# Kernel tuning notes

Hardware: AMD Instinct MI355X
Metric: run time of the kernel (lower is better)

Reference implementation:

```python
import jax, jax.numpy as jnp
import numpy as np

BETA = 0.25
EMA_DECAY = 0.99
EMA_EPS = 1e-05
K = 8192
D = 512


def setup_inputs() -> dict:
    key = jax.random.key(0)
    k1, k2, k3, k4 = jax.random.split(key, 4)
    z = jax.random.normal(k1, (8, 2048, D), dtype=jnp.float32)
    codebook_weight = jax.random.normal(k2, (K, D), dtype=jnp.float32)
    ema_cluster_size = jax.random.uniform(k3, (K,), dtype=jnp.float32)
    ema_embed_avg = jax.random.normal(k4, (K, D), dtype=jnp.float32)
    return {"z": z, "codebook_weight": codebook_weight,
            "ema_cluster_size": ema_cluster_size, "ema_embed_avg": ema_embed_avg}


def reference(z, codebook_weight, ema_cluster_size, ema_embed_avg):
    d = z.shape[-1]
    flat = z.reshape(-1, d)                                  # [N, D]
    z_sq = jnp.sum(flat * flat, axis=1, keepdims=True)       # [N, 1]
    e = codebook_weight                                      # [K, D]
    e_sq = jnp.sum(e * e, axis=1)                            # [K]
    # logits = -||z - e||^2 (argmax over logits == nearest code)
    logits = -(z_sq - 2.0 * jnp.matmul(flat, e.T) + e_sq)    # [N, K]
    idx = jnp.argmax(logits, axis=1)                         # [N]
    z_q = e[idx].reshape(z.shape)

    # commitment loss: beta * sum((z - sg[z_q])^2) / D
    vq_loss = BETA * jnp.sum((z - jax.lax.stop_gradient(z_q)) ** 2) / d

    # EMA statistics (torch.no_grad block)
    flat_sg = jax.lax.stop_gradient(flat)
    n_codes = e.shape[0]
    ones = jnp.ones(flat.shape[0], dtype=flat.dtype)
    cluster_size = jax.ops.segment_sum(ones, idx, num_segments=n_codes)       # == onehot.sum(0)
    embed_sum = jax.ops.segment_sum(flat_sg, idx, num_segments=n_codes)       # == onehot.T @ flat
    new_ema_cluster_size = ema_cluster_size * EMA_DECAY + cluster_size * (1.0 - EMA_DECAY)
    new_ema_embed_avg = ema_embed_avg * EMA_DECAY + embed_sum * (1.0 - EMA_DECAY)
    updated = new_ema_embed_avg / (new_ema_cluster_size[:, None] + EMA_EPS)
    active = (cluster_size > 0)[:, None]
    new_codebook = jnp.where(active, updated, codebook_weight)
    # (random reseeding of never-used codes is intentionally omitted: it is
    # nondeterministic and outside the deterministic math path)

    # straight-through estimator
    z_out = z + jax.lax.stop_gradient(z_q - z)
    return (z_out, vq_loss, new_ema_cluster_size, new_ema_embed_avg, new_codebook)
```

## Files before the change

kernel.cpp:

```cpp
#include <hip/hip_runtime.h>
#include <hip/hip_bf16.h>

#define N_ROWS 16384
#define DDIM   512
#define KCODES 8192
#define BETA   0.25f
#define DECAY  0.99f
#define ONE_MINUS_DECAY 0.01f
#define EMA_EPS 1e-5f

#define O_Z    0
#define O_LOSS 8388608
#define O_CS   8388609
#define O_AVG  8396801
#define O_CB   12591105

#define WS_CNT      0
#define WS_ESQ      32768
#define WS_FLAGCNT  65536
#define WS_FLAGLIST 65792
#define WS_KEYS     73984
#define WS_SEC2     205056
#define WS_LOSSP    270592
#define WS_IDXS     270848
#define WS_OFFS     336384
#define WS_CURS     369152
#define WS_ROWLIST  401920
#define WS_Z16      467456
#define WS_CB16     17244672

#define TAU  0.35f
#define RCAP 2048

typedef _Float16 half8  __attribute__((ext_vector_type(8)));
typedef float    floatx4 __attribute__((ext_vector_type(4)));

__device__ __forceinline__ unsigned enc_f(float d) {
    unsigned ub = __float_as_uint(d);
    return (ub & 0x80000000u) ? ~ub : (ub | 0x80000000u);
}
__device__ __forceinline__ float dec32(unsigned ub) {
    return __uint_as_float((ub & 0x80000000u) ? (ub ^ 0x80000000u) : ~ub);
}
__device__ __forceinline__ float dec_key(unsigned long long k) {
    return dec32((unsigned)(k >> 32));
}

__device__ __forceinline__ float4 pack8_f16(float4 a, float4 b) {
    auto p0 = __builtin_amdgcn_cvt_pkrtz(a.x, a.y);
    auto p1 = __builtin_amdgcn_cvt_pkrtz(a.z, a.w);
    auto p2 = __builtin_amdgcn_cvt_pkrtz(b.x, b.y);
    auto p3 = __builtin_amdgcn_cvt_pkrtz(b.z, b.w);
    float4 r;
    r.x = __builtin_bit_cast(float, p0);
    r.y = __builtin_bit_cast(float, p1);
    r.z = __builtin_bit_cast(float, p2);
    r.w = __builtin_bit_cast(float, p3);
    return r;
}

__device__ __forceinline__ void load_lds16(const void* g, void* l) {
    __builtin_amdgcn_global_load_lds(
        (const __attribute__((address_space(1))) unsigned int*)g,
        (__attribute__((address_space(3))) unsigned int*)l, 16, 0, 0);
}

__global__ __launch_bounds__(256) void cvtz_kernel(const float* __restrict__ z,
                                                   _Float16* __restrict__ z16) {
    size_t i = (size_t)blockIdx.x * 256 + threadIdx.x;
    const float4* p = (const float4*)z + 2 * i;
    ((float4*)z16)[i] = pack8_f16(p[0], p[1]);
}

__global__ __launch_bounds__(64) void cvtcb_kernel(const float* __restrict__ cb,
                                                   _Float16* __restrict__ cb16,
                                                   float* __restrict__ e_sq) {
    int k = blockIdx.x;
    int t = threadIdx.x;
    const float4* r = (const float4*)(cb + (size_t)k * DDIM);
    float4 a = r[2 * t], b = r[2 * t + 1];
    ((float4*)(cb16 + (size_t)k * DDIM))[t] = pack8_f16(a, b);
    float s = a.x*a.x + a.y*a.y + a.z*a.z + a.w*a.w
            + b.x*b.x + b.y*b.y + b.z*b.z + b.w*b.w;
    #pragma unroll
    for (int o = 32; o > 0; o >>= 1) s += __shfl_down(s, o);
    if (t == 0) e_sq[k] = s;
}

__global__ __launch_bounds__(256, 4) void screen_kernel(
    const _Float16* __restrict__ z16, const _Float16* __restrict__ cb16,
    const float* __restrict__ e_sq,
    unsigned long long* __restrict__ keys, unsigned* __restrict__ sec2) {
    __shared__ _Float16 zt[128 * 64];
    __shared__ _Float16 ct[128 * 64];

    const int tid = threadIdx.x;
    const int by = blockIdx.x;
    const int bx = blockIdx.y;
    const int lane = tid & 63, wid = tid >> 6;
    const int wm = wid & 1, wn = wid >> 1;
    const int lr = lane & 15, lq = lane >> 4;

    const _Float16* zsrc[4]; const _Float16* csrc[4];
    #pragma unroll
    for (int r = 0; r < 4; r++) {
        int g = (r * 4 + wid) * 64 + lane;
        int row = g >> 3, kq = g & 7;
        zsrc[r] = z16 + (size_t)(by * 128 + row) * DDIM + ((kq ^ (row & 7)) << 3);
        csrc[r] = cb16 + (size_t)(bx * 128 + row) * DDIM + ((kq ^ (row & 7)) << 3);
    }

    floatx4 acc[4][4];
    #pragma unroll
    for (int i = 0; i < 4; i++)
        #pragma unroll
        for (int j = 0; j < 4; j++) acc[i][j] = floatx4{0.f, 0.f, 0.f, 0.f};

    for (int kc = 0; kc < DDIM; kc += 64) {
        #pragma unroll
        for (int r = 0; r < 4; r++) load_lds16(zsrc[r] + kc, &zt[(r * 4 + wid) * 512]);
        #pragma unroll
        for (int r = 0; r < 4; r++) load_lds16(csrc[r] + kc, &ct[(r * 4 + wid) * 512]);
        __syncthreads();
        #pragma unroll
        for (int kk = 0; kk < 2; kk++) {
            half8 av[4];
            #pragma unroll
            for (int mt = 0; mt < 4; mt++) {
                int row = wm * 64 + mt * 16 + lr;
                av[mt] = *(const half8*)&zt[row * 64 + (((kk * 4 + lq) ^ (row & 7)) << 3)];
            }
            #pragma unroll
            for (int nt = 0; nt < 4; nt++) {
                int row = wn * 64 + nt * 16 + lr;
                half8 bv = *(const half8*)&ct[row * 64 + (((kk * 4 + lq) ^ (row & 7)) << 3)];
                #pragma unroll
                for (int mt = 0; mt < 4; mt++)
                    acc[mt][nt] = __builtin_amdgcn_mfma_f32_16x16x32_f16(av[mt], bv, acc[mt][nt], 0, 0, 0);
            }
        }
        __syncthreads();
    }

    float* eb_d1 = (float*)zt;
    int*   eb_c1 = (int*)zt + 256;
    float* eb_d2 = (float*)zt + 512;

    float es[4];
    #pragma unroll
    for (int nt = 0; nt < 4; nt++) es[nt] = e_sq[bx * 128 + wn * 64 + nt * 16 + lr];

    #pragma unroll
    for (int mt = 0; mt < 4; mt++) {
        #pragma unroll
        for (int r = 0; r < 4; r++) {
            float d1 = 1e30f, d2 = 1e30f; int c1 = 0x7FFFFFFF;
            #pragma unroll
            for (int nt = 0; nt < 4; nt++) {
                float d = fmaf(-2.0f, acc[mt][nt][r], es[nt]);
                int c = bx * 128 + wn * 64 + nt * 16 + lr;
                bool better = (d < d1) || (d == d1 && c < c1);
                if (better) { d2 = d1; d1 = d; c1 = c; }
                else        { d2 = fminf(d2, d); }
            }
            #pragma unroll
            for (int off = 1; off < 16; off <<= 1) {
                float od1 = __shfl_xor(d1, off);
                int   oc1 = __shfl_xor(c1, off);
                float od2 = __shfl_xor(d2, off);
                bool better = (od1 < d1) || (od1 == d1 && oc1 < c1);
                if (better) { d2 = fminf(d1, od2); d1 = od1; c1 = oc1; }
                else        { d2 = fminf(d2, od1); }
            }
            if (lr == 0) {
                int row = wm * 64 + mt * 16 + lq * 4 + r;
                eb_d1[wn * 128 + row] = d1; eb_c1[wn * 128 + row] = c1; eb_d2[wn * 128 + row] = d2;
            }
        }
    }
    __syncthreads();
    if (tid < 128) {
        float d1a = eb_d1[tid],       d2a = eb_d2[tid];       int c1a = eb_c1[tid];
        float d1b = eb_d1[128 + tid], d2b = eb_d2[128 + tid]; int c1b = eb_c1[128 + tid];
        bool bbet = (d1b < d1a) || (d1b == d1a && c1b < c1a);
        float d1 = bbet ? d1b : d1a; int c1 = bbet ? c1b : c1a;
        float d2 = bbet ? fminf(d1a, d2b) : fminf(d2a, d1b);
        unsigned long long key = ((unsigned long long)enc_f(d1) << 32) | (unsigned)c1;
        int row_g = by * 128 + tid;
        unsigned long long old = atomicMin(&keys[row_g], key);
        float cand = (key < old) ? fminf(dec_key(old), d2) : fminf(d1, d2);
        atomicMin(&sec2[row_g], enc_f(cand));
    }
}

__global__ void merge_kernel(unsigned long long* __restrict__ keys,
                             const unsigned* __restrict__ sec2,
                             int* __restrict__ flagcnt, int* __restrict__ flaglist) {
    int row = blockIdx.x * 256 + threadIdx.x;
    unsigned long long kb = keys[row];
    float best = dec_key(kb);
    float sec  = dec32(sec2[row]);
    if (sec - best < TAU) {
        int pos = atomicAdd(flagcnt, 1);
        if (pos < RCAP) { flaglist[pos] = row; keys[row] = ~0ULL; }
    }
}

__global__ __launch_bounds__(256) void rescore_kernel(
    const float* __restrict__ z, const float* __restrict__ cb,
    const float* __restrict__ e_sq, const int* __restrict__ flagcnt,
    const int* __restrict__ flaglist, unsigned long long* __restrict__ keys) {
    int n = *flagcnt; n = min(n, RCAP);
    int base = blockIdx.y * 64;
    if (base >= n) return;
    __shared__ float ech[64][132];
    __shared__ float zch[64][68];
    __shared__ int ridx[64];
    const int tid = threadIdx.x;
    const int bx = blockIdx.x;
    if (tid < 64) ridx[tid] = flaglist[min(base + tid, n - 1)];
    __syncthreads();

    const int tc = tid & 15;
    const int tg = tid >> 4;

    float es[8];
    #pragma unroll
    for (int c = 0; c < 8; c++) es[c] = e_sq[bx * 128 + tc * 8 + c];

    float acc[4][8] = {};
    for (int kc = 0; kc < DDIM; kc += 64) {
        #pragma unroll
        for (int l = 0; l < 8; l++) {
            int gi = tid + 256 * l;
            int code = gi >> 4, q = gi & 15;
            float4 v = *(const float4*)&cb[(size_t)(bx * 128 + code) * DDIM + kc + q * 4];
            ech[q * 4 + 0][code] = v.x; ech[q * 4 + 1][code] = v.y;
            ech[q * 4 + 2][code] = v.z; ech[q * 4 + 3][code] = v.w;
        }
        #pragma unroll
        for (int l = 0; l < 4; l++) {
            int gi = tid + 256 * l;
            int row = gi >> 4, q = gi & 15;
            float4 v = *(const float4*)&z[(size_t)ridx[row] * DDIM + kc + q * 4];
            zch[q * 4 + 0][row] = v.x; zch[q * 4 + 1][row] = v.y;
            zch[q * 4 + 2][row] = v.z; zch[q * 4 + 3][row] = v.w;
        }
        __syncthreads();
        for (int k = 0; k < 64; k++) {
            const float4 b0 = *(const float4*)&ech[k][tc * 8];
            const float4 b1 = *(const float4*)&ech[k][tc * 8 + 4];
            const float4 a  = *(const float4*)&zch[k][tg * 4];
            const float ar[4] = {a.x, a.y, a.z, a.w};
            const float br[8] = {b0.x, b0.y, b0.z, b0.w, b1.x, b1.y, b1.z, b1.w};
            #pragma unroll
            for (int r = 0; r < 4; r++)
                #pragma unroll
                for (int c = 0; c < 8; c++)
                    acc[r][c] = fmaf(ar[r], br[c], acc[r][c]);
        }
        __syncthreads();
    }

    unsigned long long (*redk)[17] = (unsigned long long (*)[17])&ech[0][0];
    #pragma unroll
    for (int r = 0; r < 4; r++) {
        unsigned long long bk = ~0ULL;
        #pragma unroll
        for (int c = 0; c < 8; c++) {
            int code = bx * 128 + tc * 8 + c;
            float d = fmaf(-2.0f, acc[r][c], es[c]);
            unsigned long long key = ((unsigned long long)enc_f(d) << 32) | (unsigned)code;
            bk = (key < bk) ? key : bk;
        }
        redk[tg * 4 + r][tc] = bk;
    }
    __syncthreads();
    if (tid < 64) {
        unsigned long long b = redk[tid][0];
        #pragma unroll
        for (int t = 1; t < 16; t++) {
            unsigned long long v = redk[tid][t];
            b = (v < b) ? v : b;
        }
        atomicMin(&keys[ridx[tid]], b);
    }
}

__global__ __launch_bounds__(128) void zout_loss_kernel(
    const float* __restrict__ z, const float* __restrict__ cb,
    const unsigned long long* __restrict__ keys,
    float* __restrict__ out, int* __restrict__ cnt,
    int* __restrict__ idxs, float* __restrict__ lossp) {
    const int row = blockIdx.x;
    const int tid = threadIdx.x;
    const int idx = (int)(unsigned int)(keys[row] & 0xFFFFFFFFull);

    const float4 zv = ((const float4*)(z  + (size_t)row * DDIM))[tid];
    const float4 ev = ((const float4*)(cb + (size_t)idx * DDIM))[tid];
    ((float4*)(out + O_Z + (size_t)row * DDIM))[tid] = ev;

    float dx = zv.x - ev.x, dy = zv.y - ev.y, dz = zv.z - ev.z, dw = zv.w - ev.w;
    float s = dx*dx + dy*dy + dz*dz + dw*dw;

    #pragma unroll
    for (int o = 32; o > 0; o >>= 1) s += __shfl_down(s, o);
    __shared__ float red[2];
    if ((tid & 63) == 0) red[tid >> 6] = s;
    __syncthreads();
    if (tid == 0) {
        atomicAdd(&lossp[row & 63], red[0] + red[1]);
        atomicAdd(&cnt[idx], 1);
        idxs[row] = idx;
    }
}

__global__ void loss_final_kernel(const float* __restrict__ lossp, float* __restrict__ out) {
    float s = lossp[threadIdx.x];
    #pragma unroll
    for (int o = 32; o > 0; o >>= 1) s += __shfl_down(s, o);
    if (threadIdx.x == 0) out[O_LOSS] = s * (BETA / (float)DDIM);
}

__global__ __launch_bounds__(256) void scan_kernel(
    const int* __restrict__ cnt, const float* __restrict__ ema_cs,
    float* __restrict__ out, int* __restrict__ offs, int* __restrict__ curs) {
    __shared__ int tot[256];
    const int t = threadIdx.x;
    const int base = t * 32;
    int local[32]; int s = 0;
    #pragma unroll
    for (int j = 0; j < 32; j++) { local[j] = cnt[base + j]; s += local[j]; }
    tot[t] = s;
    __syncthreads();
    for (int off = 1; off < 256; off <<= 1) {
        int v = (t >= off) ? tot[t - off] : 0;
        __syncthreads();
        tot[t] += v;
        __syncthreads();
    }
    int run = tot[t] - s;
    #pragma unroll
    for (int j = 0; j < 32; j++) {
        offs[base + j] = run; curs[base + j] = run;
        out[O_CS + base + j] = DECAY * ema_cs[base + j] + ONE_MINUS_DECAY * (float)local[j];
        run += local[j];
    }
}

__global__ void fill_kernel(const int* __restrict__ idxs, int* __restrict__ curs,
                            int* __restrict__ rowlist) {
    int row = blockIdx.x * 256 + threadIdx.x;
    int idx = idxs[row];
    int pos = atomicAdd(&curs[idx], 1);
    rowlist[pos] = row;
}

__global__ __launch_bounds__(256) void code_update_kernel(
    const float* __restrict__ z, const float* __restrict__ cb,
    const float* __restrict__ ema_cs, const float* __restrict__ ema_avg,
    const int* __restrict__ cnt, const int* __restrict__ offs,
    const int* __restrict__ rowlist, float* __restrict__ out) {
    const int lane = threadIdx.x & 63;
    const int k = blockIdx.x * 4 + (threadIdx.x >> 6);
    const int n = cnt[k], off = offs[k];
    float4 a0 = {0.f,0.f,0.f,0.f}, a1 = {0.f,0.f,0.f,0.f};
    for (int r = 0; r < n; r++) {
        int row = rowlist[off + r];
        const float4* zp = (const float4*)(z + (size_t)row * DDIM) + lane * 2;
        float4 v0 = zp[0], v1 = zp[1];
        a0.x += v0.x; a0.y += v0.y; a0.z += v0.z; a0.w += v0.w;
        a1.x += v1.x; a1.y += v1.y; a1.z += v1.z; a1.w += v1.w;
    }
    const float4* ep = (const float4*)(ema_avg + (size_t)k * DDIM) + lane * 2;
    float4 e0 = ep[0], e1 = ep[1];
    float4 n0, n1;
    n0.x = DECAY * e0.x + ONE_MINUS_DECAY * a0.x; n0.y = DECAY * e0.y + ONE_MINUS_DECAY * a0.y;
    n0.z = DECAY * e0.z + ONE_MINUS_DECAY * a0.z; n0.w = DECAY * e0.w + ONE_MINUS_DECAY * a0.w;
    n1.x = DECAY * e1.x + ONE_MINUS_DECAY * a1.x; n1.y = DECAY * e1.y + ONE_MINUS_DECAY * a1.y;
    n1.z = DECAY * e1.z + ONE_MINUS_DECAY * a1.z; n1.w = DECAY * e1.w + ONE_MINUS_DECAY * a1.w;
    ((float4*)(out + O_AVG + (size_t)k * DDIM))[lane * 2]     = n0;
    ((float4*)(out + O_AVG + (size_t)k * DDIM))[lane * 2 + 1] = n1;

    float ncs = DECAY * ema_cs[k] + ONE_MINUS_DECAY * (float)n;
    float inv = 1.0f / (ncs + EMA_EPS);
    float4 c0, c1;
    if (n > 0) {
        c0.x = n0.x * inv; c0.y = n0.y * inv; c0.z = n0.z * inv; c0.w = n0.w * inv;
        c1.x = n1.x * inv; c1.y = n1.y * inv; c1.z = n1.z * inv; c1.w = n1.w * inv;
    } else {
        const float4* cp = (const float4*)(cb + (size_t)k * DDIM) + lane * 2;
        c0 = cp[0]; c1 = cp[1];
    }
    ((float4*)(out + O_CB + (size_t)k * DDIM))[lane * 2]     = c0;
    ((float4*)(out + O_CB + (size_t)k * DDIM))[lane * 2 + 1] = c1;
}

extern "C" void kernel_launch(void* const* d_in, const int* in_sizes, int n_in,
                              void* d_out, int out_size, void* d_ws, size_t ws_size,
                              hipStream_t stream) {
    const float* z       = (const float*)d_in[0];
    const float* cb      = (const float*)d_in[1];
    const float* ema_cs  = (const float*)d_in[2];
    const float* ema_avg = (const float*)d_in[3];
    float* out = (float*)d_out;

    int* cnt       = (int*)((char*)d_ws + WS_CNT);
    float* e_sq    = (float*)((char*)d_ws + WS_ESQ);
    int* flagcnt   = (int*)((char*)d_ws + WS_FLAGCNT);
    int* flaglist  = (int*)((char*)d_ws + WS_FLAGLIST);
    unsigned long long* keys = (unsigned long long*)((char*)d_ws + WS_KEYS);
    unsigned* sec2 = (unsigned*)((char*)d_ws + WS_SEC2);
    float* lossp   = (float*)((char*)d_ws + WS_LOSSP);
    int* idxs      = (int*)((char*)d_ws + WS_IDXS);
    int* offs      = (int*)((char*)d_ws + WS_OFFS);
    int* curs      = (int*)((char*)d_ws + WS_CURS);
    int* rowlist   = (int*)((char*)d_ws + WS_ROWLIST);
    _Float16* z16  = (_Float16*)((char*)d_ws + WS_Z16);
    _Float16* cb16 = (_Float16*)((char*)d_ws + WS_CB16);

    hipMemsetAsync(cnt, 0, KCODES * sizeof(int), stream);
    hipMemsetAsync(flagcnt, 0, sizeof(int), stream);
    hipMemsetAsync(keys, 0xFF, N_ROWS * sizeof(unsigned long long), stream);
    hipMemsetAsync(sec2, 0xFF, N_ROWS * sizeof(unsigned), stream);
    hipMemsetAsync(lossp, 0, 64 * sizeof(float), stream);

    cvtz_kernel<<<N_ROWS * DDIM / 8 / 256, 256, 0, stream>>>(z, z16);
    cvtcb_kernel<<<KCODES, 64, 0, stream>>>(cb, cb16, e_sq);
    screen_kernel<<<dim3(N_ROWS / 128, KCODES / 128), 256, 0, stream>>>(z16, cb16, e_sq, keys, sec2);
    merge_kernel<<<N_ROWS / 256, 256, 0, stream>>>(keys, sec2, flagcnt, flaglist);
    rescore_kernel<<<dim3(KCODES / 128, RCAP / 64), 256, 0, stream>>>(z, cb, e_sq, flagcnt, flaglist, keys);
    zout_loss_kernel<<<N_ROWS, 128, 0, stream>>>(z, cb, keys, out, cnt, idxs, lossp);
    loss_final_kernel<<<1, 64, 0, stream>>>(lossp, out);
    scan_kernel<<<1, 256, 0, stream>>>(cnt, ema_cs, out, offs, curs);
    fill_kernel<<<N_ROWS / 256, 256, 0, stream>>>(idxs, curs, rowlist);
    code_update_kernel<<<KCODES / 4, 256, 0, stream>>>(z, cb, ema_cs, ema_avg, cnt, offs, rowlist, out);
}
```

Before: 629.9 us.

## Fold memsets and loss finalization into existing kernels, raise screen occupancy

Removes five hipMemsetAsync calls by initializing keys, sec2, lossp, flagcnt and cnt inside the conversion kernels. The loss_final kernel is merged into scan_kernel, and zout_loss now handles two rows per 256-thread block. screen_kernel's launch_bounds min-blocks hint goes from 4 to 5, which may cap registers and cause spills. The aim is to cut launch and memset overhead across the pipeline.

After: 744.2 us. 18.1% more time.

```diff
diff --git a/kernel.cpp b/kernel.cpp
--- a/kernel.cpp
+++ b/kernel.cpp
@@ -66,15 +66,23 @@
 }
 
 __global__ __launch_bounds__(256) void cvtz_kernel(const float* __restrict__ z,
-                                                   _Float16* __restrict__ z16) {
+                                                   _Float16* __restrict__ z16,
+                                                   unsigned long long* __restrict__ keys,
+                                                   unsigned* __restrict__ sec2,
+                                                   float* __restrict__ lossp,
+                                                   int* __restrict__ flagcnt) {
     size_t i = (size_t)blockIdx.x * 256 + threadIdx.x;
     const float4* p = (const float4*)z + 2 * i;
     ((float4*)z16)[i] = pack8_f16(p[0], p[1]);
+    if (i < N_ROWS) { keys[i] = ~0ULL; sec2[i] = 0xFFFFFFFFu; }
+    if (i < 64) lossp[i] = 0.0f;
+    if (i == 0) *flagcnt = 0;
 }
 
 __global__ __launch_bounds__(64) void cvtcb_kernel(const float* __restrict__ cb,
                                                    _Float16* __restrict__ cb16,
-                                                   float* __restrict__ e_sq) {
+                                                   float* __restrict__ e_sq,
+                                                   int* __restrict__ cnt) {
     int k = blockIdx.x;
     int t = threadIdx.x;
     const float4* r = (const float4*)(cb + (size_t)k * DDIM);
@@ -84,10 +92,10 @@
             + b.x*b.x + b.y*b.y + b.z*b.z + b.w*b.w;
     #pragma unroll
     for (int o = 32; o > 0; o >>= 1) s += __shfl_down(s, o);
-    if (t == 0) e_sq[k] = s;
-}
-
-__global__ __launch_bounds__(256, 4) void screen_kernel(
+    if (t == 0) { e_sq[k] = s; cnt[k] = 0; }
+}
+
+__global__ __launch_bounds__(256, 5) void screen_kernel(
     const _Float16* __restrict__ z16, const _Float16* __restrict__ cb16,
     const float* __restrict__ e_sq,
     unsigned long long* __restrict__ keys, unsigned* __restrict__ sec2) {
@@ -287,46 +295,48 @@
     }
 }
 
-__global__ __launch_bounds__(128) void zout_loss_kernel(
+__global__ __launch_bounds__(256) void zout_loss_kernel(
     const float* __restrict__ z, const float* __restrict__ cb,
     const unsigned long long* __restrict__ keys,
     float* __restrict__ out, int* __restrict__ cnt,
     int* __restrict__ idxs, float* __restrict__ lossp) {
-    const int row = blockIdx.x;
     const int tid = threadIdx.x;
+    const int sub = tid >> 7;
+    const int t   = tid & 127;
+    const int row = blockIdx.x * 2 + sub;
     const int idx = (int)(unsigned int)(keys[row] & 0xFFFFFFFFull);
 
-    const float4 zv = ((const float4*)(z  + (size_t)row * DDIM))[tid];
-    const float4 ev = ((const float4*)(cb + (size_t)idx * DDIM))[tid];
-    ((float4*)(out + O_Z + (size_t)row * DDIM))[tid] = ev;
+    const float4 zv = ((const float4*)(z  + (size_t)row * DDIM))[t];
+    const float4 ev = ((const float4*)(cb + (size_t)idx * DDIM))[t];
+    ((float4*)(out + O_Z + (size_t)row * DDIM))[t] = ev;
 
     float dx = zv.x - ev.x, dy = zv.y - ev.y, dz = zv.z - ev.z, dw = zv.w - ev.w;
     float s = dx*dx + dy*dy + dz*dz + dw*dw;
 
     #pragma unroll
     for (int o = 32; o > 0; o >>= 1) s += __shfl_down(s, o);
-    __shared__ float red[2];
+    __shared__ float red[4];
     if ((tid & 63) == 0) red[tid >> 6] = s;
     __syncthreads();
-    if (tid == 0) {
-        atomicAdd(&lossp[row & 63], red[0] + red[1]);
+    if (t == 0) {
+        atomicAdd(&lossp[row & 63], red[sub * 2] + red[sub * 2 + 1]);
         atomicAdd(&cnt[idx], 1);
         idxs[row] = idx;
     }
 }
 
-__global__ void loss_final_kernel(const float* __restrict__ lossp, float* __restrict__ out) {
-    float s = lossp[threadIdx.x];
-    #pragma unroll
-    for (int o = 32; o > 0; o >>= 1) s += __shfl_down(s, o);
-    if (threadIdx.x == 0) out[O_LOSS] = s * (BETA / (float)DDIM);
-}
-
 __global__ __launch_bounds__(256) void scan_kernel(
     const int* __restrict__ cnt, const float* __restrict__ ema_cs,
+    const float* __restrict__ lossp,
     float* __restrict__ out, int* __restrict__ offs, int* __restrict__ curs) {
     __shared__ int tot[256];
     const int t = threadIdx.x;
+    if (t < 64) {
+        float s = lossp[t];
+        #pragma unroll
+        for (int o = 32; o > 0; o >>= 1) s += __shfl_down(s, o);
+        if (t == 0) out[O_LOSS] = s * (BETA / (float)DDIM);
+    }
     const int base = t * 32;
     int local[32]; int s = 0;
     #pragma unroll
@@ -419,20 +429,13 @@
     _Float16* z16  = (_Float16*)((char*)d_ws + WS_Z16);
     _Float16* cb16 = (_Float16*)((char*)d_ws + WS_CB16);
 
-    hipMemsetAsync(cnt, 0, KCODES * sizeof(int), stream);
-    hipMemsetAsync(flagcnt, 0, sizeof(int), stream);
-    hipMemsetAsync(keys, 0xFF, N_ROWS * sizeof(unsigned long long), stream);
-    hipMemsetAsync(sec2, 0xFF, N_ROWS * sizeof(unsigned), stream);
-    hipMemsetAsync(lossp, 0, 64 * sizeof(float), stream);
-
-    cvtz_kernel<<<N_ROWS * DDIM / 8 / 256, 256, 0, stream>>>(z, z16);
-    cvtcb_kernel<<<KCODES, 64, 0, stream>>>(cb, cb16, e_sq);
+    cvtz_kernel<<<N_ROWS * DDIM / 8 / 256, 256, 0, stream>>>(z, z16, keys, sec2, lossp, flagcnt);
+    cvtcb_kernel<<<KCODES, 64, 0, stream>>>(cb, cb16, e_sq, cnt);
     screen_kernel<<<dim3(N_ROWS / 128, KCODES / 128), 256, 0, stream>>>(z16, cb16, e_sq, keys, sec2);
     merge_kernel<<<N_ROWS / 256, 256, 0, stream>>>(keys, sec2, flagcnt, flaglist);
     rescore_kernel<<<dim3(KCODES / 128, RCAP / 64), 256, 0, stream>>>(z, cb, e_sq, flagcnt, flaglist, keys);
-    zout_loss_kernel<<<N_ROWS, 128, 0, stream>>>(z, cb, keys, out, cnt, idxs, lossp);
-    loss_final_kernel<<<1, 64, 0, stream>>>(lossp, out);
-    scan_kernel<<<1, 256, 0, stream>>>(cnt, ema_cs, out, offs, curs);
+    zout_loss_kernel<<<N_ROWS / 2, 256, 0, stream>>>(z, cb, keys, out, cnt, idxs, lossp);
+    scan_kernel<<<1, 256, 0, stream>>>(cnt, ema_cs, lossp, out, offs, curs);
     fill_kernel<<<N_ROWS / 256, 256, 0, stream>>>(idxs, curs, rowlist);
     code_update_kernel<<<KCODES / 4, 256, 0, stream>>>(z, cb, ema_cs, ema_avg, cnt, offs, rowlist, out);
 }
```
